# Performance work log

Hardware: AMD Instinct MI355X
Metric: run time of the kernel (lower is better)

## Reference

```python
import jax, jax.numpy as jnp
import numpy as np

B, N, C = 8, 1024, 1024
H = 16
D = C // H  # head_dim = 64
SCALE = D ** -0.5


def setup_inputs() -> dict:
    key = jax.random.key(0)
    k1, k2, k3, k4 = jax.random.split(key, 4)
    x = jax.random.normal(k1, (B, N, C), dtype=jnp.float32)
    qkv_w = jax.random.normal(k2, (3 * C, C), dtype=jnp.float32) * (C ** -0.5)
    proj_w = jax.random.normal(k3, (C, C), dtype=jnp.float32) * (C ** -0.5)
    proj_b = jax.random.normal(k4, (C,), dtype=jnp.float32)
    return {"x": x, "qkv_w": qkv_w, "proj_w": proj_w, "proj_b": proj_b}


def reference(x, qkv_w, proj_w, proj_b):
    # qkv projection: torch Linear weight is [out, in] -> x @ W^T
    qkv = jnp.einsum('bnc,oc->bno', x, qkv_w)            # [B, N, 3C]
    qkv = qkv.reshape(B, N, 3, H, D)
    q = jnp.transpose(qkv[:, :, 0], (0, 2, 1, 3))        # [B, H, N, D]
    k = jnp.transpose(qkv[:, :, 1], (0, 2, 1, 3))
    v = jnp.transpose(qkv[:, :, 2], (0, 2, 1, 3))
    attn = jnp.einsum('bhqd,bhkd->bhqk', q, k) * SCALE   # [B, H, N, N]
    attn = jax.nn.softmax(attn, axis=-1)
    out = jnp.einsum('bhqk,bhkd->bhqd', attn, v)         # [B, H, N, D]
    out = jnp.transpose(out, (0, 2, 1, 3)).reshape(B, N, C)
    out = jnp.einsum('bnc,oc->bno', out, proj_w) + proj_b
    return out
```

## Files before the change

kernel.cpp:

```cpp
#include <hip/hip_runtime.h>
#include <hip/hip_bf16.h>
#include <stdint.h>

#define B_ 8
#define N_ 1024
#define C_ 1024
#define H_ 16

static constexpr float SCALE = 0.125f;
static constexpr float LOG2E = 1.4426950408889634f;
static constexpr float SL    = SCALE * LOG2E;

typedef __attribute__((ext_vector_type(4))) float f32x4;
typedef __attribute__((ext_vector_type(8))) short s16x8;

__device__ __forceinline__ ushort f2bf(float f) {
    union { float f; uint32_t u; } c; c.f = f;
    uint32_t u = c.u;
    return (ushort)((u + 0x7fffu + ((u >> 16) & 1u)) >> 16);
}

__device__ __forceinline__ ushort f2bfc(float f) {
    union { __hip_bfloat16 h; ushort u; } c;
    c.h = __float2bfloat16(f);
    return c.u;
}

__device__ __forceinline__ void gload_lds16(const void* g, void* l) {
    __builtin_amdgcn_global_load_lds(
        (const __attribute__((address_space(1))) void*)g,
        (__attribute__((address_space(3))) void*)l,
        16, 0, 0);
}
__device__ __forceinline__ void gload_lds4(const void* g, void* l) {
    __builtin_amdgcn_global_load_lds(
        (const __attribute__((address_space(1))) void*)g,
        (__attribute__((address_space(3))) void*)l,
        4, 0, 0);
}

__global__ __launch_bounds__(256) void cvt_all(const float* __restrict__ x,
                                               const float* __restrict__ qkv_w,
                                               const float* __restrict__ proj_w,
                                               ushort* __restrict__ xb,
                                               ushort* __restrict__ wqkv,
                                               ushort* __restrict__ wproj) {
    int i = blockIdx.x * 256 + threadIdx.x;
    const float* src;
    ushort* dst;
    float sc = 1.0f;
    if (i < 2097152) {
        src = x; dst = xb;
    } else if (i < 2097152 + 786432) {
        i -= 2097152;
        src = qkv_w; dst = wqkv;
        if (i < 262144) sc = SL;
    } else {
        i -= 2097152 + 786432;
        src = proj_w; dst = wproj;
    }
    float4 v = ((const float4*)src)[i];
    ushort4 o = make_ushort4(f2bf(v.x * sc), f2bf(v.y * sc), f2bf(v.z * sc), f2bf(v.w * sc));
    ((ushort4*)dst)[i] = o;
}

template<int OUT_BF16>
__global__ __launch_bounds__(256) void gemm_bt(const ushort* __restrict__ A,
                                               const ushort* __restrict__ Bw,
                                               void* __restrict__ Cout,
                                               const float* __restrict__ bias,
                                               int M, int Nout, int K) {
    __shared__ ushort Asm[128 * 64];
    __shared__ ushort Bsm[128 * 64];
    const int t = threadIdx.x;
    const int l = t & 63, w = t >> 6;
    const int lq = l & 15, lg = l >> 4;

    int bid = blockIdx.y * gridDim.x + blockIdx.x;
    const int cpx = (gridDim.x * gridDim.y) >> 3;
    bid = (bid & 7) * cpx + (bid >> 3);
    const int trow = (bid / gridDim.x) * 128, tcol = (bid % gridDim.x) * 128;

    const int wrow = (w >> 1) * 64, wcol = (w & 1) * 64;

    f32x4 acc[4][4] = {};

    const int srow0 = t >> 3;
    const int sc8 = (((t & 7) ^ (srow0 & 7)) * 8);
    const size_t abase = (size_t)(trow + srow0) * K + sc8;
    const size_t bbase = (size_t)(tcol + srow0) * K + sc8;

    for (int k0 = 0; k0 < K; k0 += 64) {
#pragma unroll
        for (int i = 0; i < 4; ++i) {
            gload_lds16(A + abase + (size_t)i * 32 * K + k0, &Asm[(i * 256 + w * 64) * 8]);
            gload_lds16(Bw + bbase + (size_t)i * 32 * K + k0, &Bsm[(i * 256 + w * 64) * 8]);
        }
        __syncthreads();
#pragma unroll
        for (int kk = 0; kk < 2; ++kk) {
            s16x8 af[4], bf[4];
#pragma unroll
            for (int m = 0; m < 4; ++m) {
                int row = wrow + m * 16 + lq;
                int ch = (kk * 4 + lg) ^ (row & 7);
                af[m] = *(const s16x8*)&Asm[row * 64 + ch * 8];
            }
#pragma unroll
            for (int n = 0; n < 4; ++n) {
                int row = wcol + n * 16 + lq;
                int ch = (kk * 4 + lg) ^ (row & 7);
                bf[n] = *(const s16x8*)&Bsm[row * 64 + ch * 8];
            }
#pragma unroll
            for (int m = 0; m < 4; ++m)
#pragma unroll
                for (int n = 0; n < 4; ++n)
                    acc[m][n] = __builtin_amdgcn_mfma_f32_16x16x32_bf16(af[m], bf[n], acc[m][n], 0, 0, 0);
        }
        __syncthreads();
    }

#pragma unroll
    for (int m = 0; m < 4; ++m)
#pragma unroll
        for (int n = 0; n < 4; ++n)
#pragma unroll
            for (int r = 0; r < 4; ++r) {
                int row = trow + wrow + m * 16 + lg * 4 + r;
                int col = tcol + wcol + n * 16 + lq;
                if (OUT_BF16) {
                    ((ushort*)Cout)[(size_t)row * Nout + col] = f2bfc(acc[m][n][r]);
                } else {
                    ((float*)Cout)[(size_t)row * Nout + col] = acc[m][n][r] + bias[col];
                }
            }
}

__global__ __launch_bounds__(512, 2) void gemm_bt256(const ushort* __restrict__ A,
                                                     const ushort* __restrict__ Bw,
                                                     ushort* __restrict__ Cout,
                                                     int M, int Nout, int K) {
    __shared__ ushort Asm[2][256 * 64];
    __shared__ ushort Bsm[2][256 * 64];
    const int t = threadIdx.x;
    const int l = t & 63, w = t >> 6;
    const int lq = l & 15, lg = l >> 4;
    const int wm = w >> 2, wn = w & 3;

    int bid = blockIdx.y * gridDim.x + blockIdx.x;
    const int cpx = (gridDim.x * gridDim.y) >> 3;
    bid = (bid & 7) * cpx + (bid >> 3);
    const int bx = bid % gridDim.x, by = bid / gridDim.x;
    const int trow = by * 256, tcol = bx * 256;

    f32x4 acc[8][4] = {};

    const int srow = t >> 3;
    const int scc = ((t & 7) ^ (srow & 7)) * 8;
    const size_t abase = (size_t)(trow + srow) * K + scc;
    const size_t bbase = (size_t)(tcol + srow) * K + scc;

#define STAGE256(buf, k0)                                                      \
    {                                                                          \
        _Pragma("unroll")                                                      \
        for (int j = 0; j < 4; ++j) {                                          \
            gload_lds16(A + abase + (size_t)j * 64 * K + (k0),                 \
                        &Asm[buf][(j * 512 + t) * 8]);                         \
            gload_lds16(Bw + bbase + (size_t)j * 64 * K + (k0),                \
                        &Bsm[buf][(j * 512 + t) * 8]);                         \
        }                                                                      \
    }
#define LOADA(dst, qr, kk)                                                     \
    _Pragma("unroll") for (int m = 0; m < 4; ++m) {                            \
        const int row = wm * 128 + (qr) * 64 + m * 16 + lq;                    \
        dst[m] = *(const s16x8*)&Asm[cur][row * 64 +                           \
                        ((((kk) * 4 + lg) ^ (row & 7)) * 8)];                  \
    }
#define LOADB(dst, qc, kk)                                                     \
    _Pragma("unroll") for (int n = 0; n < 2; ++n) {                            \
        const int row = wn * 64 + (qc) * 32 + n * 16 + lq;                     \
        dst[n] = *(const s16x8*)&Bsm[cur][row * 64 +                           \
                        ((((kk) * 4 + lg) ^ (row & 7)) * 8)];                  \
    }
#define MFMA8(qr, qc, aset, bset)                                              \
    _Pragma("unroll") for (int m = 0; m < 4; ++m)                              \
        _Pragma("unroll") for (int n = 0; n < 2; ++n)                          \
            acc[(qr) * 4 + m][(qc) * 2 + n] =                                  \
                __builtin_amdgcn_mfma_f32_16x16x32_bf16(                       \
                    aset[m], bset[n], acc[(qr) * 4 + m][(qc) * 2 + n], 0,0,0);

    STAGE256(0, 0);
    asm volatile("s_waitcnt vmcnt(0)" ::: "memory");
    __builtin_amdgcn_s_barrier();

    const int NT = K / 64;
    for (int kt = 0; kt < NT; ++kt) {
        const int cur = kt & 1, nxt = cur ^ 1;
        s16x8 a00[4], a10[4], a11[4], a01[4];
        s16x8 b00[2], b10[2], b01[2], b11[2];
        if (kt < NT - 1) STAGE256(nxt, (kt + 1) * 64);
        LOADA(a00, 0, 0); LOADB(b00, 0, 0); LOADB(b10, 1, 0);
        LOADA(a10, 1, 0);                       MFMA8(0, 0, a00, b00);
        LOADA(a11, 1, 1); LOADB(b01, 0, 1);     MFMA8(0, 1, a00, b10);
        LOADB(b11, 1, 1);                       MFMA8(1, 1, a10, b10);
        LOADA(a01, 0, 1);                       MFMA8(1, 0, a10, b00);
                                                MFMA8(1, 0, a11, b01);
                                                MFMA8(1, 1, a11, b11);
                                                MFMA8(0, 1, a01, b11);
                                                MFMA8(0, 0, a01, b01);
        asm volatile("s_waitcnt vmcnt(0)" ::: "memory");
        __builtin_amdgcn_s_barrier();
    }

#pragma unroll
    for (int mt = 0; mt < 8; ++mt)
#pragma unroll
        for (int nt = 0; nt < 4; ++nt)
#pragma unroll
            for (int r = 0; r < 4; ++r) {
                int row = trow + wm * 128 + mt * 16 + lg * 4 + r;
                int col = tcol + wn * 64 + nt * 16 + lq;
                Cout[(size_t)row * Nout + col] = f2bfc(acc[mt][nt][r]);
            }
#undef STAGE256
#undef LOADA
#undef LOADB
#undef MFMA8
}

__global__ __launch_bounds__(512, 4) void attn_fwd(const ushort* __restrict__ qk,
                                                   const ushort* __restrict__ vt,
                                                   ushort* __restrict__ attn_out) {
    __shared__ ushort Klds[64 * 64];
    __shared__ ushort Vlds[64 * 64];

    const int t = threadIdx.x, l = t & 63, w = t >> 6;
    const int lq = l & 15, lg = l >> 4;

    const int serial = blockIdx.x + 4 * blockIdx.y;
    const int logical = (serial & 7) * 64 + (serial >> 3);
    const int qt = logical & 3;
    const int bh = logical >> 2;
    const int b = bh >> 4, h = bh & 15;

    const int qbase = qt * 256 + w * 32 + lq;
    const size_t qoff0 = (size_t)(b * N_ + qbase) * 2048 + h * 64;
    const size_t qoff1 = qoff0 + (size_t)16 * 2048;
    const s16x8 qa0 = *(const s16x8*)&qk[qoff0 + lg * 8];
    const s16x8 qa1 = *(const s16x8*)&qk[qoff0 + 32 + lg * 8];
    const s16x8 qb0 = *(const s16x8*)&qk[qoff1 + lg * 8];
    const s16x8 qb1 = *(const s16x8*)&qk[qoff1 + 32 + lg * 8];

    float lr0 = 0.f, lr1 = 0.f;
    f32x4 o0[4] = {}, o1[4] = {};

    const int srow0 = t >> 3;
    const int sc8 = ((t & 7) ^ (srow0 & 7)) * 8;
    const size_t kgbase = (size_t)(b * N_ + srow0) * 2048 + 1024 + h * 64 + sc8;

    const ushort* vptr[4];
#pragma unroll
    for (int j = 0; j < 4; ++j) {
        const int d = 8 * w + 2 * j + (l >> 5);
        const int c = ((l & 31) >> 2) ^ (d & 7);
        const int s = c * 8 + (l & 3) * 2;
        const int key = (s >> 5) * 32 + ((s >> 2) & 1) * 16 + ((s >> 3) & 3) * 4 + (s & 3);
        vptr[j] = vt + (size_t)(h * 64 + d) * (B_ * N_) + b * N_ + key;
    }

    for (int kt = 0; kt < N_ / 64; ++kt) {
        gload_lds16(qk + kgbase + (size_t)kt * 64 * 2048, &Klds[w * 512]);
#pragma unroll
        for (int j = 0; j < 4; ++j)
            gload_lds4(vptr[j] + kt * 64, &Vlds[w * 512 + j * 128]);
        __syncthreads();

        f32x4 s0[4], s1[4];
#pragma unroll
        for (int g = 0; g < 4; ++g) {
            int key = g * 16 + lq;
            const s16x8 kf0 = *(const s16x8*)&Klds[key * 64 + ((lg ^ (key & 7)) * 8)];
            const s16x8 kf1 = *(const s16x8*)&Klds[key * 64 + (((4 + lg) ^ (key & 7)) * 8)];
            f32x4 z0 = {}, z1 = {};
            z0    = __builtin_amdgcn_mfma_f32_16x16x32_bf16(kf0, qa0, z0, 0, 0, 0);
            s0[g] = __builtin_amdgcn_mfma_f32_16x16x32_bf16(kf1, qa1, z0, 0, 0, 0);
            z1    = __builtin_amdgcn_mfma_f32_16x16x32_bf16(kf0, qb0, z1, 0, 0, 0);
            s1[g] = __builtin_amdgcn_mfma_f32_16x16x32_bf16(kf1, qb1, z1, 0, 0, 0);
        }

#pragma unroll
        for (int kb = 0; kb < 2; ++kb) {
            s16x8 pf0, pf1;
#pragma unroll
            for (int i = 0; i < 4; ++i) {
                float a0 = __builtin_amdgcn_exp2f(s0[2 * kb][i]);
                float a1 = __builtin_amdgcn_exp2f(s0[2 * kb + 1][i]);
                float b0 = __builtin_amdgcn_exp2f(s1[2 * kb][i]);
                float b1 = __builtin_amdgcn_exp2f(s1[2 * kb + 1][i]);
                lr0 += a0 + a1;
                lr1 += b0 + b1;
                pf0[i] = (short)f2bfc(a0); pf0[4 + i] = (short)f2bfc(a1);
                pf1[i] = (short)f2bfc(b0); pf1[4 + i] = (short)f2bfc(b1);
            }
#pragma unroll
            for (int ds = 0; ds < 4; ++ds) {
                const s16x8 vf = *(const s16x8*)
                    &Vlds[(ds * 16 + lq) * 64 + (((kb * 4 + lg) ^ (lq & 7)) * 8)];
                o0[ds] = __builtin_amdgcn_mfma_f32_16x16x32_bf16(pf0, vf, o0[ds], 0, 0, 0);
                o1[ds] = __builtin_amdgcn_mfma_f32_16x16x32_bf16(pf1, vf, o1[ds], 0, 0, 0);
            }
        }
        __syncthreads();
    }

    lr0 += __shfl_xor(lr0, 16); lr0 += __shfl_xor(lr0, 32);
    lr1 += __shfl_xor(lr1, 16); lr1 += __shfl_xor(lr1, 32);

#pragma unroll
    for (int r = 0; r < 4; ++r) {
        float rl0 = 1.f / __shfl(lr0, lg * 4 + r);
        float rl1 = 1.f / __shfl(lr1, lg * 4 + r);
        int orow = qt * 256 + w * 32 + lg * 4 + r;
        size_t base0 = (size_t)(b * N_ + orow) * C_ + h * 64 + lq;
        size_t base1 = base0 + (size_t)16 * C_;
#pragma unroll
        for (int ds = 0; ds < 4; ++ds) {
            attn_out[base0 + ds * 16] = f2bfc(o0[ds][r] * rl0);
            attn_out[base1 + ds * 16] = f2bfc(o1[ds][r] * rl1);
        }
    }
}

extern "C" void kernel_launch(void* const* d_in, const int* in_sizes, int n_in,
                              void* d_out, int out_size, void* d_ws, size_t ws_size,
                              hipStream_t stream) {
    const float* x      = (const float*)d_in[0];
    const float* qkv_w  = (const float*)d_in[1];
    const float* proj_w = (const float*)d_in[2];
    const float* proj_b = (const float*)d_in[3];
    float* out = (float*)d_out;

    ushort* ws    = (ushort*)d_ws;
    ushort* xb    = ws;
    ushort* wqkv  = xb + (size_t)8192 * 1024;
    ushort* wproj = wqkv + (size_t)3072 * 1024;
    ushort* qkb   = wproj + (size_t)1024 * 1024;
    ushort* vtb   = qkb + (size_t)8192 * 2048;
    ushort* attn  = vtb + (size_t)1024 * 8192;

    cvt_all<<<12288, 256, 0, stream>>>(x, qkv_w, proj_w, xb, wqkv, wproj);

    gemm_bt256<<<dim3(8, 32), 512, 0, stream>>>(xb, wqkv, qkb, 8192, 2048, 1024);
    gemm_bt<1><<<dim3(64, 8), 256, 0, stream>>>(wqkv + (size_t)2048 * 1024, xb, (void*)vtb,
                                                nullptr, 1024, 8192, 1024);

    attn_fwd<<<dim3(4, 128), 512, 0, stream>>>(qkb, vtb, attn);

    gemm_bt<0><<<dim3(8, 64), 256, 0, stream>>>(attn, wproj, (void*)out, proj_b, 8192, 1024, 1024);
}
```

Before: 142.1 us.

## Enlarge attention query tile to 64 rows per wave for K/V reuse

Each wave in the attention kernel now handles 64 query rows instead of 32, so a block covers 512 queries and the grid is halved to 256 blocks. Every K/V tile staged in LDS is reused across twice as many MFMAs, which halves global K/V traffic and LDS fill/sync overhead per unit of work. The cost is more accumulator and Q registers per thread, so launch bounds drop to 2 blocks per CU. With only 256 blocks on a 256-CU part, latency hiding and load balance may suffer.

```diff
diff --git a/kernel.cpp b/kernel.cpp
--- a/kernel.cpp
+++ b/kernel.cpp
@@ -229,7 +229,7 @@
 #undef MFMA8
 }
 
-__global__ __launch_bounds__(512, 4) void attn_fwd(const ushort* __restrict__ qk,
+__global__ __launch_bounds__(512, 2) void attn_fwd(const ushort* __restrict__ qk,
                                                    const ushort* __restrict__ vt,
                                                    ushort* __restrict__ attn_out) {
     __shared__ ushort Klds[64 * 64];
@@ -238,22 +238,23 @@
     const int t = threadIdx.x, l = t & 63, w = t >> 6;
     const int lq = l & 15, lg = l >> 4;
 
-    const int serial = blockIdx.x + 4 * blockIdx.y;
-    const int logical = (serial & 7) * 64 + (serial >> 3);
-    const int qt = logical & 3;
-    const int bh = logical >> 2;
+    const int serial = blockIdx.x + 2 * blockIdx.y;
+    const int logical = (serial & 7) * 32 + (serial >> 3);
+    const int qt = logical & 1;
+    const int bh = logical >> 1;
     const int b = bh >> 4, h = bh & 15;
 
-    const int qbase = qt * 256 + w * 32 + lq;
-    const size_t qoff0 = (size_t)(b * N_ + qbase) * 2048 + h * 64;
-    const size_t qoff1 = qoff0 + (size_t)16 * 2048;
-    const s16x8 qa0 = *(const s16x8*)&qk[qoff0 + lg * 8];
-    const s16x8 qa1 = *(const s16x8*)&qk[qoff0 + 32 + lg * 8];
-    const s16x8 qb0 = *(const s16x8*)&qk[qoff1 + lg * 8];
-    const s16x8 qb1 = *(const s16x8*)&qk[qoff1 + 32 + lg * 8];
-
-    float lr0 = 0.f, lr1 = 0.f;
-    f32x4 o0[4] = {}, o1[4] = {};
+    const int qbase = qt * 512 + w * 64 + lq;
+    s16x8 qf[4][2];
+#pragma unroll
+    for (int sub = 0; sub < 4; ++sub) {
+        const size_t qo = (size_t)(b * N_ + qbase + sub * 16) * 2048 + h * 64;
+        qf[sub][0] = *(const s16x8*)&qk[qo + lg * 8];
+        qf[sub][1] = *(const s16x8*)&qk[qo + 32 + lg * 8];
+    }
+
+    float lr[4] = {0.f, 0.f, 0.f, 0.f};
+    f32x4 o[4][4] = {};
 
     const int srow0 = t >> 3;
     const int sc8 = ((t & 7) ^ (srow0 & 7)) * 8;
@@ -276,60 +277,62 @@
             gload_lds4(vptr[j] + kt * 64, &Vlds[w * 512 + j * 128]);
         __syncthreads();
 
-        f32x4 s0[4], s1[4];
-#pragma unroll
-        for (int g = 0; g < 4; ++g) {
-            int key = g * 16 + lq;
-            const s16x8 kf0 = *(const s16x8*)&Klds[key * 64 + ((lg ^ (key & 7)) * 8)];
-            const s16x8 kf1 = *(const s16x8*)&Klds[key * 64 + (((4 + lg) ^ (key & 7)) * 8)];
-            f32x4 z0 = {}, z1 = {};
-            z0    = __builtin_amdgcn_mfma_f32_16x16x32_bf16(kf0, qa0, z0, 0, 0, 0);
-            s0[g] = __builtin_amdgcn_mfma_f32_16x16x32_bf16(kf1, qa1, z0, 0, 0, 0);
-            z1    = __builtin_amdgcn_mfma_f32_16x16x32_bf16(kf0, qb0, z1, 0, 0, 0);
-            s1[g] = __builtin_amdgcn_mfma_f32_16x16x32_bf16(kf1, qb1, z1, 0, 0, 0);
-        }
-
-#pragma unroll
-        for (int kb = 0; kb < 2; ++kb) {
-            s16x8 pf0, pf1;
-#pragma unroll
-            for (int i = 0; i < 4; ++i) {
-                float a0 = __builtin_amdgcn_exp2f(s0[2 * kb][i]);
-                float a1 = __builtin_amdgcn_exp2f(s0[2 * kb + 1][i]);
-                float b0 = __builtin_amdgcn_exp2f(s1[2 * kb][i]);
-                float b1 = __builtin_amdgcn_exp2f(s1[2 * kb + 1][i]);
-                lr0 += a0 + a1;
-                lr1 += b0 + b1;
-                pf0[i] = (short)f2bfc(a0); pf0[4 + i] = (short)f2bfc(a1);
-                pf1[i] = (short)f2bfc(b0); pf1[4 + i] = (short)f2bfc(b1);
+#pragma unroll
+        for (int gp = 0; gp < 2; ++gp) {
+            f32x4 s[2][4];
+#pragma unroll
+            for (int g2 = 0; g2 < 2; ++g2) {
+                const int key = (gp * 2 + g2) * 16 + lq;
+                const s16x8 kf0 = *(const s16x8*)&Klds[key * 64 + ((lg ^ (key & 7)) * 8)];
+                const s16x8 kf1 = *(const s16x8*)&Klds[key * 64 + (((4 + lg) ^ (key & 7)) * 8)];
+#pragma unroll
+                for (int sub = 0; sub < 4; ++sub) {
+                    f32x4 z = {};
+                    z = __builtin_amdgcn_mfma_f32_16x16x32_bf16(kf0, qf[sub][0], z, 0, 0, 0);
+                    s[g2][sub] = __builtin_amdgcn_mfma_f32_16x16x32_bf16(kf1, qf[sub][1], z, 0, 0, 0);
+                }
+            }
+            s16x8 pfr[4];
+#pragma unroll
+            for (int sub = 0; sub < 4; ++sub) {
+#pragma unroll
+                for (int i = 0; i < 4; ++i) {
+                    float a0 = __builtin_amdgcn_exp2f(s[0][sub][i]);
+                    float a1 = __builtin_amdgcn_exp2f(s[1][sub][i]);
+                    lr[sub] += a0 + a1;
+                    pfr[sub][i]     = (short)f2bfc(a0);
+                    pfr[sub][4 + i] = (short)f2bfc(a1);
+                }
             }
 #pragma unroll
             for (int ds = 0; ds < 4; ++ds) {
                 const s16x8 vf = *(const s16x8*)
-                    &Vlds[(ds * 16 + lq) * 64 + (((kb * 4 + lg) ^ (lq & 7)) * 8)];
-                o0[ds] = __builtin_amdgcn_mfma_f32_16x16x32_bf16(pf0, vf, o0[ds], 0, 0, 0);
-                o1[ds] = __builtin_amdgcn_mfma_f32_16x16x32_bf16(pf1, vf, o1[ds], 0, 0, 0);
+                    &Vlds[(ds * 16 + lq) * 64 + (((gp * 4 + lg) ^ (lq & 7)) * 8)];
+#pragma unroll
+                for (int sub = 0; sub < 4; ++sub)
+                    o[sub][ds] = __builtin_amdgcn_mfma_f32_16x16x32_bf16(pfr[sub], vf, o[sub][ds], 0, 0, 0);
             }
         }
         __syncthreads();
     }
 
-    lr0 += __shfl_xor(lr0, 16); lr0 += __shfl_xor(lr0, 32);
-    lr1 += __shfl_xor(lr1, 16); lr1 += __shfl_xor(lr1, 32);
-
-#pragma unroll
-    for (int r = 0; r < 4; ++r) {
-        float rl0 = 1.f / __shfl(lr0, lg * 4 + r);
-        float rl1 = 1.f / __shfl(lr1, lg * 4 + r);
-        int orow = qt * 256 + w * 32 + lg * 4 + r;
-        size_t base0 = (size_t)(b * N_ + orow) * C_ + h * 64 + lq;
-        size_t base1 = base0 + (size_t)16 * C_;
-#pragma unroll
-        for (int ds = 0; ds < 4; ++ds) {
-            attn_out[base0 + ds * 16] = f2bfc(o0[ds][r] * rl0);
-            attn_out[base1 + ds * 16] = f2bfc(o1[ds][r] * rl1);
+#pragma unroll
+    for (int sub = 0; sub < 4; ++sub) {
+        lr[sub] += __shfl_xor(lr[sub], 16);
+        lr[sub] += __shfl_xor(lr[sub], 32);
+    }
+
+#pragma unroll
+    for (int sub = 0; sub < 4; ++sub)
+#pragma unroll
+        for (int r = 0; r < 4; ++r) {
+            float rl = 1.f / __shfl(lr[sub], lg * 4 + r);
+            int orow = qt * 512 + w * 64 + sub * 16 + lg * 4 + r;
+            size_t base = (size_t)(b * N_ + orow) * C_ + h * 64 + lq;
+#pragma unroll
+            for (int ds = 0; ds < 4; ++ds)
+                attn_out[base + ds * 16] = f2bfc(o[sub][ds][r] * rl);
         }
-    }
 }
 
 extern "C" void kernel_launch(void* const* d_in, const int* in_sizes, int n_in,
@@ -355,7 +358,7 @@
     gemm_bt<1><<<dim3(64, 8), 256, 0, stream>>>(wqkv + (size_t)2048 * 1024, xb, (void*)vtb,
                                                 nullptr, 1024, 8192, 1024);
 
-    attn_fwd<<<dim3(4, 128), 512, 0, stream>>>(qkb, vtb, attn);
+    attn_fwd<<<dim3(2, 128), 512, 0, stream>>>(qkb, vtb, attn);
 
     gemm_bt<0><<<dim3(8, 64), 256, 0, stream>>>(attn, wproj, (void*)out, proj_b, 8192, 1024, 1024);
 }
```

New measurement: 143.4 us. About the same (+0.9%).
